# Performance work log

Measured on AMD Instinct MI355X. Metric: run time of the kernel, lower is better.

The kernel has to match this reference:

```python
import jax, jax.numpy as jnp
import numpy as np

HIDDEN = 512
HEADS = 8
NORM = 1.0 / np.sqrt(HIDDEN // HEADS)  # torch: 1/sqrt(tensor(dim_k)//head) = 1/8


def setup_inputs() -> dict:
    key = jax.random.key(0)
    ks = jax.random.split(key, 14)
    B, N, D = 2, 2048, HIDDEN
    s = 0.02
    d = {
        "x_re": jax.random.normal(ks[0], (B, N, D), dtype=jnp.float32),
        "x_im": jax.random.normal(ks[1], (B, N, D), dtype=jnp.float32),
    }
    names = ["Wq_re", "Wq_im", "bq_re", "bq_im",
             "Wk_re", "Wk_im", "bk_re", "bk_im",
             "Wv_re", "Wv_im", "bv_re", "bv_im"]
    for i, nm in enumerate(names):
        shape = (D, D) if nm.startswith("W") else (D,)
        d[nm] = jax.random.normal(ks[2 + i], shape, dtype=jnp.float32) * s
    return d


def reference(x_re, x_im,
              Wq_re, Wq_im, bq_re, bq_im,
              Wk_re, Wk_im, bk_re, bk_im,
              Wv_re, Wv_im, bv_re, bv_im):
    B, N, D = x_re.shape
    h, dk = HEADS, D // HEADS
    x = jax.lax.complex(x_re, x_im)
    Wq = jax.lax.complex(Wq_re, Wq_im); bq = jax.lax.complex(bq_re, bq_im)
    Wk = jax.lax.complex(Wk_re, Wk_im); bk = jax.lax.complex(bk_re, bk_im)
    Wv = jax.lax.complex(Wv_re, Wv_im); bv = jax.lax.complex(bv_re, bv_im)

    def proj(W, b):  # torch nn.Linear: x @ W.T + b, then split heads -> [B,h,N,dk]
        y = x @ W.T + b
        return y.reshape(B, N, h, dk).transpose(0, 2, 1, 3)

    q, k, v = proj(Wq, bq), proj(Wk, bk), proj(Wv, bv)
    # complex matmul (no conjugation, matching torch.matmul), scaled
    dist = jnp.einsum("bhnd,bhmd->bhnm", q, k) * NORM
    probs = jax.nn.softmax(jnp.abs(dist), axis=-1).astype(jnp.complex64)
    att = jnp.einsum("bhnm,bhmd->bhnd", probs, v)
    att = att.transpose(0, 2, 1, 3).reshape(B, N, D)
    # real-view output [B, N, D, 2]
    return jnp.stack([att.real, att.imag], axis=-1)
```

## Files before the change

### kernel.cpp

```cpp
#include <hip/hip_runtime.h>
#include <hip/hip_bf16.h>
#include <math.h>

#define B_ 2
#define N_ 2048
#define D_ 512
#define H_ 8
#define DK_ 64
#define M_ (B_ * N_)

typedef short s16x8 __attribute__((ext_vector_type(8)));
typedef short s16x4 __attribute__((ext_vector_type(4)));
typedef float fx4   __attribute__((ext_vector_type(4)));
typedef int   ix4   __attribute__((ext_vector_type(4)));

static __device__ __forceinline__ short f2bf(float f) {
    __hip_bfloat16 h = __float2bfloat16(f);
    return __builtin_bit_cast(short, h);
}
static __device__ __forceinline__ float bf2f(short s) {
    unsigned int u = ((unsigned int)(unsigned short)s) << 16;
    return __builtin_bit_cast(float, u);
}
static __device__ __forceinline__ float fexp2(float x) {
#if __has_builtin(__builtin_amdgcn_exp2f)
    return __builtin_amdgcn_exp2f(x);
#else
    return exp2f(x);
#endif
}
static __device__ __forceinline__ float fsqrt_(float x) {
#if __has_builtin(__builtin_amdgcn_sqrtf)
    return __builtin_amdgcn_sqrtf(x);
#else
    return sqrtf(x);
#endif
}
static __device__ __forceinline__ int pack_tr(float a, float b) {
    unsigned ua = __builtin_bit_cast(unsigned, a);
    unsigned ub = __builtin_bit_cast(unsigned, b);
    return (int)((ua >> 16) | (ub & 0xFFFF0000u));
}

#define MFMA16(a, b, c) __builtin_amdgcn_mfma_f32_16x16x32_bf16(a, b, c, 0, 0, 0)

#define C2_ 0.18033688f
#define M0_ 16.0f

__global__ __launch_bounds__(256, 2)
void qkproj_mfma(const float* __restrict__ xr, const float* __restrict__ xi,
                 const float* __restrict__ W0r, const float* __restrict__ W0i,
                 const float* __restrict__ b0r, const float* __restrict__ b0i,
                 const float* __restrict__ W1r, const float* __restrict__ W1i,
                 const float* __restrict__ b1r, const float* __restrict__ b1i,
                 short* __restrict__ o0r, short* __restrict__ o0i,
                 short* __restrict__ o1r, short* __restrict__ o1i)
{
    __shared__ short sA[2][128][40];
    __shared__ short sB[2][64][40];

    const int tid = threadIdx.x;
    const int w = tid >> 6, l = tid & 63, lg = l >> 4, lc = l & 15;
    const int wr = w >> 1, wc = w & 1;
    const int bn = blockIdx.x, bm = blockIdx.y, z = blockIdx.z;
    const float* Wr = z ? W1r : W0r;
    const float* Wi = z ? W1i : W0i;
    const float* br = z ? b1r : b0r;
    const float* bi = z ? b1i : b0i;
    short* outr = z ? o1r : o0r;
    short* outi = z ? o1i : o0i;

    const int srow = tid >> 3, scol = (tid & 7) * 4;
    int aoff = (bm * 128 + srow) * D_ + scol;
    int boff = (bn * 64 + srow) * D_ + scol;

    float4 rA[8], rB[4];
    auto issue = [&]() {
#pragma unroll
        for (int u = 0; u < 8; ++u) {
            const float* src = (u >= 4) ? xi : xr;
            rA[u] = *(const float4*)&src[aoff + (u & 3) * 32 * D_];
        }
#pragma unroll
        for (int u = 0; u < 4; ++u) {
            const float* src = (u >= 2) ? Wi : Wr;
            rB[u] = *(const float4*)&src[boff + (u & 1) * 32 * D_];
        }
        aoff += 32; boff += 32;
    };

    fx4 Cre[4][2], Cim[4][2];
#pragma unroll
    for (int mf = 0; mf < 4; ++mf)
#pragma unroll
        for (int nf = 0; nf < 2; ++nf)
#pragma unroll
            for (int j = 0; j < 4; ++j) { Cre[mf][nf][j] = 0.f; Cim[mf][nf][j] = 0.f; }

    issue();
    for (int k0 = 0; k0 < D_; k0 += 32) {
        __syncthreads();
#pragma unroll
        for (int u = 0; u < 8; ++u) {
            int comp = u >> 2, row = (u & 3) * 32 + srow;
            float vv[4] = {rA[u].x, rA[u].y, rA[u].z, rA[u].w};
            s16x4 hv;
#pragma unroll
            for (int q = 0; q < 4; ++q) hv[q] = f2bf(vv[q]);
            *(s16x4*)&sA[comp][row][scol] = hv;
        }
#pragma unroll
        for (int u = 0; u < 4; ++u) {
            int comp = u >> 1, row = (u & 1) * 32 + srow;
            float vv[4] = {rB[u].x, rB[u].y, rB[u].z, rB[u].w};
            s16x4 hv;
#pragma unroll
            for (int q = 0; q < 4; ++q) hv[q] = f2bf(vv[q]);
            *(s16x4*)&sB[comp][row][scol] = hv;
        }
        __syncthreads();
        if (k0 + 32 < D_) issue();

        s16x8 a[2][4];
#pragma unroll
        for (int comp = 0; comp < 2; ++comp)
#pragma unroll
            for (int mf = 0; mf < 4; ++mf)
                a[comp][mf] = *(const s16x8*)&sA[comp][wr * 64 + mf * 16 + lc][lg * 8];
        s16x8 bfr[2][2], bin[2];
#pragma unroll
        for (int comp = 0; comp < 2; ++comp)
#pragma unroll
            for (int nf = 0; nf < 2; ++nf)
                bfr[comp][nf] = *(const s16x8*)&sB[comp][wc * 32 + nf * 16 + lc][lg * 8];
#pragma unroll
        for (int nf = 0; nf < 2; ++nf) bin[nf] = bfr[1][nf] ^ (short)0x8000;

        __builtin_amdgcn_s_setprio(1);
#pragma unroll
        for (int mf = 0; mf < 4; ++mf)
#pragma unroll
            for (int nf = 0; nf < 2; ++nf) {
                Cre[mf][nf] = MFMA16(a[0][mf], bfr[0][nf], Cre[mf][nf]);
                Cre[mf][nf] = MFMA16(a[1][mf], bin[nf],    Cre[mf][nf]);
                Cim[mf][nf] = MFMA16(a[0][mf], bfr[1][nf], Cim[mf][nf]);
                Cim[mf][nf] = MFMA16(a[1][mf], bfr[0][nf], Cim[mf][nf]);
            }
        __builtin_amdgcn_s_setprio(0);
    }

    const int bb = (bm * 128) >> 11;
#pragma unroll
    for (int nf = 0; nf < 2; ++nf) {
        const int c = bn * 64 + wc * 32 + nf * 16 + lc;
        const float brv = br[c], biv = bi[c];
        const int h = c >> 6, dd = c & 63;
        const int n00 = (bm * 128 + wr * 64 + lg * 4) & (N_ - 1);
        size_t obase = (((size_t)(bb * H_ + h) * N_) + n00) * DK_ + dd;
#pragma unroll
        for (int mf = 0; mf < 4; ++mf)
#pragma unroll
            for (int j = 0; j < 4; ++j) {
                size_t o = obase + (size_t)(mf * 16 + j) * DK_;
                outr[o] = f2bf(Cre[mf][nf][j] + brv);
                outi[o] = f2bf(Cim[mf][nf][j] + biv);
            }
    }
}

__global__ __launch_bounds__(256, 2)
void vproj_mfma(const float* __restrict__ xr, const float* __restrict__ xi,
                const float* __restrict__ Wr, const float* __restrict__ Wi,
                const float* __restrict__ br, const float* __restrict__ bi,
                short* __restrict__ outr, short* __restrict__ outi)
{
    __shared__ short sA[2][2][64][40];
    __shared__ short sB[2][2][64][40];

    const int tid = threadIdx.x;
    const int w = tid >> 6, l = tid & 63, lg = l >> 4, lc = l & 15;
    const int wr = w >> 1, wc = w & 1;
    const int bn = blockIdx.x, bm = blockIdx.y;

    const int srow = tid >> 3, scol = (tid & 7) * 4;
    int aoff = (bm * 64 + srow) * D_ + scol;
    int boff = (bn * 64 + srow) * D_ + scol;

    float4 rA[4], rB[4];
    auto issue = [&]() {
#pragma unroll
        for (int u = 0; u < 4; ++u) {
            const float* src = (u >= 2) ? xi : xr;
            rA[u] = *(const float4*)&src[aoff + (u & 1) * 32 * D_];
        }
#pragma unroll
        for (int u = 0; u < 4; ++u) {
            const float* src = (u >= 2) ? Wi : Wr;
            rB[u] = *(const float4*)&src[boff + (u & 1) * 32 * D_];
        }
        aoff += 32; boff += 32;
    };

    fx4 Cre[2][2], Cim[2][2];
#pragma unroll
    for (int mf = 0; mf < 2; ++mf)
#pragma unroll
        for (int nf = 0; nf < 2; ++nf)
#pragma unroll
            for (int j = 0; j < 4; ++j) { Cre[mf][nf][j] = 0.f; Cim[mf][nf][j] = 0.f; }

    issue();
    for (int k0 = 0; k0 < D_; k0 += 32) {
        __syncthreads();
#pragma unroll
        for (int u = 0; u < 4; ++u) {
            int comp = u >> 1, row = (u & 1) * 32 + srow;
            float vv[4] = {rA[u].x, rA[u].y, rA[u].z, rA[u].w};
            s16x4 hv, lv;
#pragma unroll
            for (int q = 0; q < 4; ++q) {
                short hh = f2bf(vv[q]);
                hv[q] = hh;
                lv[q] = f2bf(vv[q] - bf2f(hh));
            }
            *(s16x4*)&sA[comp][0][row][scol] = hv;
            *(s16x4*)&sA[comp][1][row][scol] = lv;
        }
#pragma unroll
        for (int u = 0; u < 4; ++u) {
            int comp = u >> 1, row = (u & 1) * 32 + srow;
            float vv[4] = {rB[u].x, rB[u].y, rB[u].z, rB[u].w};
            s16x4 hv, lv;
#pragma unroll
            for (int q = 0; q < 4; ++q) {
                short hh = f2bf(vv[q]);
                hv[q] = hh;
                lv[q] = f2bf(vv[q] - bf2f(hh));
            }
            *(s16x4*)&sB[comp][0][row][scol] = hv;
            *(s16x4*)&sB[comp][1][row][scol] = lv;
        }
        __syncthreads();
        if (k0 + 32 < D_) issue();

        s16x8 a[2][2][2];
#pragma unroll
        for (int comp = 0; comp < 2; ++comp)
#pragma unroll
            for (int s = 0; s < 2; ++s)
#pragma unroll
                for (int mf = 0; mf < 2; ++mf)
                    a[comp][s][mf] = *(const s16x8*)&sA[comp][s][wr * 32 + mf * 16 + lc][lg * 8];
        s16x8 bfr[2][2][2], bin[2][2];
#pragma unroll
        for (int comp = 0; comp < 2; ++comp)
#pragma unroll
            for (int s = 0; s < 2; ++s)
#pragma unroll
                for (int nf = 0; nf < 2; ++nf)
                    bfr[comp][s][nf] = *(const s16x8*)&sB[comp][s][wc * 32 + nf * 16 + lc][lg * 8];
#pragma unroll
        for (int s = 0; s < 2; ++s)
#pragma unroll
            for (int nf = 0; nf < 2; ++nf)
                bin[s][nf] = bfr[1][s][nf] ^ (short)0x8000;

        __builtin_amdgcn_s_setprio(1);
#pragma unroll
        for (int mf = 0; mf < 2; ++mf)
#pragma unroll
            for (int nf = 0; nf < 2; ++nf) {
                fx4 cr = Cre[mf][nf], ci = Cim[mf][nf];
                cr = MFMA16(a[0][0][mf], bfr[0][0][nf], cr);
                cr = MFMA16(a[1][0][mf], bin[0][nf],    cr);
                ci = MFMA16(a[0][0][mf], bfr[1][0][nf], ci);
                ci = MFMA16(a[1][0][mf], bfr[0][0][nf], ci);
                cr = MFMA16(a[0][0][mf], bfr[0][1][nf], cr);
                cr = MFMA16(a[0][1][mf], bfr[0][0][nf], cr);
                cr = MFMA16(a[1][0][mf], bin[1][nf],    cr);
                cr = MFMA16(a[1][1][mf], bin[0][nf],    cr);
                ci = MFMA16(a[0][0][mf], bfr[1][1][nf], ci);
                ci = MFMA16(a[0][1][mf], bfr[1][0][nf], ci);
                ci = MFMA16(a[1][0][mf], bfr[0][1][nf], ci);
                ci = MFMA16(a[1][1][mf], bfr[0][0][nf], ci);
                Cre[mf][nf] = cr; Cim[mf][nf] = ci;
            }
        __builtin_amdgcn_s_setprio(0);
    }

    const int bb = (bm * 64) >> 11;
#pragma unroll
    for (int nf = 0; nf < 2; ++nf) {
        const int c = bn * 64 + wc * 32 + nf * 16 + lc;
        const float brv = br[c], biv = bi[c];
        const int h = c >> 6, dd = c & 63;
#pragma unroll
        for (int mf = 0; mf < 2; ++mf) {
            int m0 = bm * 64 + wr * 32 + mf * 16 + lg * 4;
            int n0 = m0 & (N_ - 1);
            s16x4 pr, pi;
#pragma unroll
            for (int j = 0; j < 4; ++j) {
                pr[j] = f2bf(Cre[mf][nf][j] + brv);
                pi[j] = f2bf(Cim[mf][nf][j] + biv);
            }
            size_t o = (((size_t)(bb * H_ + h) * DK_) + dd) * N_ + n0;
            *(s16x4*)&outr[o] = pr;
            *(s16x4*)&outi[o] = pi;
        }
    }
}

#define NT_ (N_ / 64)
#define NR_ (NT_ / 2)

static __device__ __forceinline__ int swz8(int row, int slot) {
    return (slot + (row & 7) + 2 * ((row >> 3) & 3)) & 7;
}

__global__ __launch_bounds__(512, 2)
void attn_mfma(const short* __restrict__ qr, const short* __restrict__ qi,
               const short* __restrict__ kr, const short* __restrict__ ki,
               const short* __restrict__ vtr, const short* __restrict__ vti,
               float* __restrict__ out)
{
    __shared__ short sK [2][2][2][64][64];
    __shared__ short sVt[2][2][2][64][64];

    const int tid = threadIdx.x;
    const int w = tid >> 6, l = tid & 63, lg = l >> 4, lc = l & 15;
    const int kg = w & 1, qw = w >> 1;

    const int dlin = blockIdx.y * 16 + blockIdx.x;
    const int xcd = dlin & 7, slot = dlin >> 3;
    const int bh = xcd * 2 + (slot >> 4);
    const int qt = slot & 15;
    const int b = bh >> 3, h = bh & 7;

    s16x8 Qr[2][2], Qi_[2][2], Qin[2][2];
#pragma unroll
    for (int qh = 0; qh < 2; ++qh) {
        size_t base = ((size_t)bh * N_ + (size_t)qt * 128 + qw * 32 + qh * 16 + lc) * DK_ + lg * 8;
#pragma unroll
        for (int c = 0; c < 2; ++c) {
            Qr[qh][c]  = *(const s16x8*)&qr[base + c * 32];
            Qi_[qh][c] = *(const s16x8*)&qi[base + c * 32];
            Qin[qh][c] = Qi_[qh][c] ^ (short)0x8000;
        }
    }

    s16x8 onesf;
#pragma unroll
    for (int u = 0; u < 8; ++u) onesf[u] = (short)0x3F80;

    fx4 o_re[2][4], o_im[2][4], o_l[2];
#pragma unroll
    for (int qh = 0; qh < 2; ++qh) {
#pragma unroll
        for (int dt = 0; dt < 4; ++dt)
#pragma unroll
            for (int j = 0; j < 4; ++j) { o_re[qh][dt][j] = 0.f; o_im[qh][dt][j] = 0.f; }
#pragma unroll
        for (int j = 0; j < 4; ++j) o_l[qh][j] = 0.f;
    }

    const int rS = ((lc >> 2) << 3) | (lc & 3);
    const int bqs = lg + (lc & 3) + 2 * (lc >> 2);
    const int bvs = lg + (lc & 7) + 2 * (lc >> 3);

    const int srow = tid >> 3, cs = tid & 7;
    const int sw = swz8(srow, cs) * 8;
    int koff = bh * (N_ * DK_) + srow * DK_ + cs * 8;
    int voff = bh * (DK_ * N_) + srow * N_ + cs * 8;

    s16x8 rgK[2][2], rgV[2][2];
    auto issue = [&]() {
#pragma unroll
        for (int g = 0; g < 2; ++g) {
            rgK[g][0] = *(const s16x8*)&kr [koff + g * 64 * DK_];
            rgK[g][1] = *(const s16x8*)&ki [koff + g * 64 * DK_];
            rgV[g][0] = *(const s16x8*)&vtr[voff + g * 64];
            rgV[g][1] = *(const s16x8*)&vti[voff + g * 64];
        }
        koff += 128 * DK_; voff += 128;
    };
    auto stage = [&](int nb) {
#pragma unroll
        for (int g = 0; g < 2; ++g)
#pragma unroll
            for (int comp = 0; comp < 2; ++comp) {
                *(s16x8*)&sK [nb][g][comp][srow][sw] = rgK[g][comp];
                *(s16x8*)&sVt[nb][g][comp][srow][sw] = rgV[g][comp];
            }
    };

    issue();
    stage(0);
    for (int r = 0; r < NR_; ++r) {
        const int cb = r & 1;
        __syncthreads();
        if (r + 1 < NR_) issue();

        fx4 are[2][4], aim[2][4];
#pragma unroll
        for (int qh = 0; qh < 2; ++qh)
#pragma unroll
            for (int t = 0; t < 4; ++t)
#pragma unroll
                for (int j = 0; j < 4; ++j) { are[qh][t][j] = 0.f; aim[qh][t][j] = 0.f; }

        __builtin_amdgcn_s_setprio(1);
#pragma unroll
        for (int t = 0; t < 4; ++t) {
            const int row = rS + ((t & 1) << 2) + ((t >> 1) << 5);
#pragma unroll
            for (int c = 0; c < 2; ++c) {
                const int sl = ((bqs + 4 * ((c + t) & 1)) & 7) * 8;
                s16x8 Krf = *(const s16x8*)&sK[cb][kg][0][row][sl];
                s16x8 Kif = *(const s16x8*)&sK[cb][kg][1][row][sl];
#pragma unroll
                for (int qh = 0; qh < 2; ++qh) {
                    are[qh][t] = MFMA16(Krf, Qr[qh][c],  are[qh][t]);
                    are[qh][t] = MFMA16(Kif, Qin[qh][c], are[qh][t]);
                    aim[qh][t] = MFMA16(Kif, Qr[qh][c],  aim[qh][t]);
                    aim[qh][t] = MFMA16(Krf, Qi_[qh][c], aim[qh][t]);
                }
            }
        }
        __builtin_amdgcn_s_setprio(0);

        s16x8 Pf[2][2];
#pragma unroll
        for (int qh = 0; qh < 2; ++qh) {
            ix4 w0, w1;
#pragma unroll
            for (int t = 0; t < 4; ++t) {
                float p[4];
#pragma unroll
                for (int j = 0; j < 4; ++j) {
                    float u2 = fmaf(are[qh][t][j], are[qh][t][j], aim[qh][t][j] * aim[qh][t][j]);
                    p[j] = fexp2(fmaf(C2_, fsqrt_(u2), -M0_));
                }
                int d0 = pack_tr(p[0], p[1]);
                int d1 = pack_tr(p[2], p[3]);
                if (t == 0)      { w0[0] = d0; w0[1] = d1; }
                else if (t == 1) { w0[2] = d0; w0[3] = d1; }
                else if (t == 2) { w1[0] = d0; w1[1] = d1; }
                else             { w1[2] = d0; w1[3] = d1; }
            }
            Pf[qh][0] = __builtin_bit_cast(s16x8, w0);
            Pf[qh][1] = __builtin_bit_cast(s16x8, w1);
        }

        __builtin_amdgcn_s_setprio(1);
#pragma unroll
        for (int qh = 0; qh < 2; ++qh) {
            o_l[qh] = MFMA16(Pf[qh][0], onesf, o_l[qh]);
            o_l[qh] = MFMA16(Pf[qh][1], onesf, o_l[qh]);
        }
#pragma unroll
        for (int dt = 0; dt < 4; ++dt) {
            const int d = dt * 16 + lc;
            const int s0 = ((bvs + 4 * dt) & 7) * 8;
            const int s1 = ((bvs + 4 * dt + 4) & 7) * 8;
            s16x8 Vr0 = *(const s16x8*)&sVt[cb][kg][0][d][s0];
            s16x8 Vi0 = *(const s16x8*)&sVt[cb][kg][1][d][s0];
            s16x8 Vr1 = *(const s16x8*)&sVt[cb][kg][0][d][s1];
            s16x8 Vi1 = *(const s16x8*)&sVt[cb][kg][1][d][s1];
#pragma unroll
            for (int qh = 0; qh < 2; ++qh) {
                o_re[qh][dt] = MFMA16(Pf[qh][0], Vr0, o_re[qh][dt]);
                o_im[qh][dt] = MFMA16(Pf[qh][0], Vi0, o_im[qh][dt]);
                o_re[qh][dt] = MFMA16(Pf[qh][1], Vr1, o_re[qh][dt]);
                o_im[qh][dt] = MFMA16(Pf[qh][1], Vi1, o_im[qh][dt]);
            }
        }
        __builtin_amdgcn_s_setprio(0);

        if (r + 1 < NR_) stage(cb ^ 1);
    }

    float* red = (float*)&sK[0][0][0][0][0];
    float2* po = (float2*)out;
#pragma unroll
    for (int qh = 0; qh < 2; ++qh) {
        __syncthreads();
        if (kg == 1) {
            const int base = (qw * 64 + l) * 37;
#pragma unroll
            for (int dt = 0; dt < 4; ++dt)
#pragma unroll
                for (int j = 0; j < 4; ++j) {
                    red[base + dt * 8 + j * 2 + 0] = o_re[qh][dt][j];
                    red[base + dt * 8 + j * 2 + 1] = o_im[qh][dt][j];
                }
#pragma unroll
            for (int j = 0; j < 4; ++j) red[base + 32 + j] = o_l[qh][j];
        }
        __syncthreads();
        if (kg == 0) {
            const int base = (qw * 64 + l) * 37;
            float inv[4];
#pragma unroll
            for (int j = 0; j < 4; ++j)
                inv[j] = 1.f / (o_l[qh][j] + red[base + 32 + j]);
#pragma unroll
            for (int dt = 0; dt < 4; ++dt)
#pragma unroll
                for (int j = 0; j < 4; ++j) {
                    float re = o_re[qh][dt][j] + red[base + dt * 8 + j * 2 + 0];
                    float im = o_im[qh][dt][j] + red[base + dt * 8 + j * 2 + 1];
                    int n  = qt * 128 + qw * 32 + qh * 16 + lg * 4 + j;
                    int dg = h * 64 + dt * 16 + lc;
                    po[((size_t)b * N_ + n) * D_ + dg] =
                        make_float2(re * inv[j], im * inv[j]);
                }
        }
    }
}

extern "C" void kernel_launch(void* const* d_in, const int* in_sizes, int n_in,
                              void* d_out, int out_size, void* d_ws, size_t ws_size,
                              hipStream_t stream)
{
    const float* xr = (const float*)d_in[0];
    const float* xi = (const float*)d_in[1];
    const float* Wq_r = (const float*)d_in[2];
    const float* Wq_i = (const float*)d_in[3];
    const float* bq_r = (const float*)d_in[4];
    const float* bq_i = (const float*)d_in[5];
    const float* Wk_r = (const float*)d_in[6];
    const float* Wk_i = (const float*)d_in[7];
    const float* bk_r = (const float*)d_in[8];
    const float* bk_i = (const float*)d_in[9];
    const float* Wv_r = (const float*)d_in[10];
    const float* Wv_i = (const float*)d_in[11];
    const float* bv_r = (const float*)d_in[12];
    const float* bv_i = (const float*)d_in[13];

    short* ws = (short*)d_ws;
    const size_t SZ = (size_t)B_ * H_ * N_ * DK_;
    short* qr_  = ws + 0 * SZ;
    short* qi_  = ws + 1 * SZ;
    short* kr_  = ws + 2 * SZ;
    short* ki_  = ws + 3 * SZ;
    short* vtr_ = ws + 4 * SZ;
    short* vti_ = ws + 5 * SZ;

    dim3 qkgrid(D_ / 64, M_ / 128, 2);
    qkproj_mfma<<<qkgrid, 256, 0, stream>>>(xr, xi,
                                            Wq_r, Wq_i, bq_r, bq_i,
                                            Wk_r, Wk_i, bk_r, bk_i,
                                            qr_, qi_, kr_, ki_);
    dim3 vgrid(D_ / 64, M_ / 64);
    vproj_mfma<<<vgrid, 256, 0, stream>>>(xr, xi, Wv_r, Wv_i, bv_r, bv_i, vtr_, vti_);

    dim3 agrid(16, 16);
    attn_mfma<<<agrid, 512, 0, stream>>>(qr_, qi_, kr_, ki_, vtr_, vti_, (float*)d_out);
}
```

Baseline: 120.7 us.

## Software-pipeline QK^T of next tile with softmax and PV of previous tile

Restructures the attention main loop into a skewed pipeline. The K-tile score MFMAs for iteration r are interleaved with the exp/pack of iteration r-1's magnitudes and its PV MFMAs, with K and V loads and staging split and offset by one iteration. A prologue and epilogue handle the first score tile and the final PV. The aim is to overlap transcendental VALU work with MFMA work to hide softmax latency, at the cost of extra live registers (the u2 array) and more complex buffer indexing.

After: 161.0 us. 33.5% more time.

```diff
diff --git a/kernel.cpp b/kernel.cpp
--- a/kernel.cpp
+++ b/kernel.cpp
@@ -374,33 +374,44 @@
     int voff = bh * (DK_ * N_) + srow * N_ + cs * 8;
 
     s16x8 rgK[2][2], rgV[2][2];
-    auto issue = [&]() {
+    auto issueK = [&]() {
 #pragma unroll
         for (int g = 0; g < 2; ++g) {
-            rgK[g][0] = *(const s16x8*)&kr [koff + g * 64 * DK_];
-            rgK[g][1] = *(const s16x8*)&ki [koff + g * 64 * DK_];
+            rgK[g][0] = *(const s16x8*)&kr[koff + g * 64 * DK_];
+            rgK[g][1] = *(const s16x8*)&ki[koff + g * 64 * DK_];
+        }
+        koff += 128 * DK_;
+    };
+    auto issueV = [&]() {
+#pragma unroll
+        for (int g = 0; g < 2; ++g) {
             rgV[g][0] = *(const s16x8*)&vtr[voff + g * 64];
             rgV[g][1] = *(const s16x8*)&vti[voff + g * 64];
         }
-        koff += 128 * DK_; voff += 128;
+        voff += 128;
     };
-    auto stage = [&](int nb) {
+    auto stageK = [&](int nb) {
 #pragma unroll
         for (int g = 0; g < 2; ++g)
 #pragma unroll
-            for (int comp = 0; comp < 2; ++comp) {
-                *(s16x8*)&sK [nb][g][comp][srow][sw] = rgK[g][comp];
+            for (int comp = 0; comp < 2; ++comp)
+                *(s16x8*)&sK[nb][g][comp][srow][sw] = rgK[g][comp];
+    };
+    auto stageV = [&](int nb) {
+#pragma unroll
+        for (int g = 0; g < 2; ++g)
+#pragma unroll
+            for (int comp = 0; comp < 2; ++comp)
                 *(s16x8*)&sVt[nb][g][comp][srow][sw] = rgV[g][comp];
-            }
     };
 
-    issue();
-    stage(0);
-    for (int r = 0; r < NR_; ++r) {
-        const int cb = r & 1;
-        __syncthreads();
-        if (r + 1 < NR_) issue();
-
+    fx4 u2[2][4];
+
+    issueK(); issueV();
+    stageK(0); stageV(0);
+    issueK(); issueV();
+    __syncthreads();
+    {
         fx4 are[2][4], aim[2][4];
 #pragma unroll
         for (int qh = 0; qh < 2; ++qh)
@@ -408,7 +419,6 @@
             for (int t = 0; t < 4; ++t)
 #pragma unroll
                 for (int j = 0; j < 4; ++j) { are[qh][t][j] = 0.f; aim[qh][t][j] = 0.f; }
-
         __builtin_amdgcn_s_setprio(1);
 #pragma unroll
         for (int t = 0; t < 4; ++t) {
@@ -416,8 +426,8 @@
 #pragma unroll
             for (int c = 0; c < 2; ++c) {
                 const int sl = ((bqs + 4 * ((c + t) & 1)) & 7) * 8;
-                s16x8 Krf = *(const s16x8*)&sK[cb][kg][0][row][sl];
-                s16x8 Kif = *(const s16x8*)&sK[cb][kg][1][row][sl];
+                s16x8 Krf = *(const s16x8*)&sK[0][kg][0][row][sl];
+                s16x8 Kif = *(const s16x8*)&sK[0][kg][1][row][sl];
 #pragma unroll
                 for (int qh = 0; qh < 2; ++qh) {
                     are[qh][t] = MFMA16(Krf, Qr[qh][c],  are[qh][t]);
@@ -428,30 +438,74 @@
             }
         }
         __builtin_amdgcn_s_setprio(0);
-
-        s16x8 Pf[2][2];
-#pragma unroll
-        for (int qh = 0; qh < 2; ++qh) {
-            ix4 w0, w1;
-#pragma unroll
-            for (int t = 0; t < 4; ++t) {
+#pragma unroll
+        for (int qh = 0; qh < 2; ++qh)
+#pragma unroll
+            for (int t = 0; t < 4; ++t)
+#pragma unroll
+                for (int j = 0; j < 4; ++j)
+                    u2[qh][t][j] = fmaf(are[qh][t][j], are[qh][t][j],
+                                        aim[qh][t][j] * aim[qh][t][j]);
+        stageK(1);
+    }
+
+    for (int r = 1; r < NR_; ++r) {
+        const int cb = r & 1;
+        __syncthreads();
+        if (r + 1 < NR_) issueK();
+        stageV(cb);
+        if (r + 1 < NR_) issueV();
+
+        fx4 are[2][4], aim[2][4];
+#pragma unroll
+        for (int qh = 0; qh < 2; ++qh)
+#pragma unroll
+            for (int t = 0; t < 4; ++t)
+#pragma unroll
+                for (int j = 0; j < 4; ++j) { are[qh][t][j] = 0.f; aim[qh][t][j] = 0.f; }
+
+        ix4 wA[2], wB[2];
+        __builtin_amdgcn_s_setprio(1);
+#pragma unroll
+        for (int t = 0; t < 4; ++t) {
+            const int row = rS + ((t & 1) << 2) + ((t >> 1) << 5);
+#pragma unroll
+            for (int c = 0; c < 2; ++c) {
+                const int sl = ((bqs + 4 * ((c + t) & 1)) & 7) * 8;
+                s16x8 Krf = *(const s16x8*)&sK[cb][kg][0][row][sl];
+                s16x8 Kif = *(const s16x8*)&sK[cb][kg][1][row][sl];
+#pragma unroll
+                for (int qh = 0; qh < 2; ++qh) {
+                    are[qh][t] = MFMA16(Krf, Qr[qh][c],  are[qh][t]);
+                    are[qh][t] = MFMA16(Kif, Qin[qh][c], are[qh][t]);
+                    aim[qh][t] = MFMA16(Kif, Qr[qh][c],  aim[qh][t]);
+                    aim[qh][t] = MFMA16(Krf, Qi_[qh][c], aim[qh][t]);
+                }
+            }
+#pragma unroll
+            for (int qh = 0; qh < 2; ++qh) {
                 float p[4];
 #pragma unroll
-                for (int j = 0; j < 4; ++j) {
-                    float u2 = fmaf(are[qh][t][j], are[qh][t][j], aim[qh][t][j] * aim[qh][t][j]);
-                    p[j] = fexp2(fmaf(C2_, fsqrt_(u2), -M0_));
-                }
+                for (int j = 0; j < 4; ++j)
+                    p[j] = fexp2(fmaf(C2_, fsqrt_(u2[qh][t][j]), -M0_));
                 int d0 = pack_tr(p[0], p[1]);
                 int d1 = pack_tr(p[2], p[3]);
-                if (t == 0)      { w0[0] = d0; w0[1] = d1; }
-                else if (t == 1) { w0[2] = d0; w0[3] = d1; }
-                else if (t == 2) { w1[0] = d0; w1[1] = d1; }
-                else             { w1[2] = d0; w1[3] = d1; }
-            }
-            Pf[qh][0] = __builtin_bit_cast(s16x8, w0);
-            Pf[qh][1] = __builtin_bit_cast(s16x8, w1);
-        }
-
+                if (t == 0)      { wA[qh][0] = d0; wA[qh][1] = d1; }
+                else if (t == 1) { wA[qh][2] = d0; wA[qh][3] = d1; }
+                else if (t == 2) { wB[qh][0] = d0; wB[qh][1] = d1; }
+                else             { wB[qh][2] = d0; wB[qh][3] = d1; }
+            }
+        }
+        __builtin_amdgcn_s_setprio(0);
+
+        s16x8 Pf[2][2];
+#pragma unroll
+        for (int qh = 0; qh < 2; ++qh) {
+            Pf[qh][0] = __builtin_bit_cast(s16x8, wA[qh]);
+            Pf[qh][1] = __builtin_bit_cast(s16x8, wB[qh]);
+        }
+
+        const int vb = cb ^ 1;
         __builtin_amdgcn_s_setprio(1);
 #pragma unroll
         for (int qh = 0; qh < 2; ++qh) {
@@ -463,10 +517,10 @@
             const int d = dt * 16 + lc;
             const int s0 = ((bvs + 4 * dt) & 7) * 8;
             const int s1 = ((bvs + 4 * dt + 4) & 7) * 8;
-            s16x8 Vr0 = *(const s16x8*)&sVt[cb][kg][0][d][s0];
-            s16x8 Vi0 = *(const s16x8*)&sVt[cb][kg][1][d][s0];
-            s16x8 Vr1 = *(const s16x8*)&sVt[cb][kg][0][d][s1];
-            s16x8 Vi1 = *(const s16x8*)&sVt[cb][kg][1][d][s1];
+            s16x8 Vr0 = *(const s16x8*)&sVt[vb][kg][0][d][s0];
+            s16x8 Vi0 = *(const s16x8*)&sVt[vb][kg][1][d][s0];
+            s16x8 Vr1 = *(const s16x8*)&sVt[vb][kg][0][d][s1];
+            s16x8 Vi1 = *(const s16x8*)&sVt[vb][kg][1][d][s1];
 #pragma unroll
             for (int qh = 0; qh < 2; ++qh) {
                 o_re[qh][dt] = MFMA16(Pf[qh][0], Vr0, o_re[qh][dt]);
@@ -474,10 +528,67 @@
                 o_re[qh][dt] = MFMA16(Pf[qh][1], Vr1, o_re[qh][dt]);
                 o_im[qh][dt] = MFMA16(Pf[qh][1], Vi1, o_im[qh][dt]);
             }
+#pragma unroll
+            for (int qh = 0; qh < 2; ++qh)
+#pragma unroll
+                for (int j = 0; j < 4; ++j)
+                    u2[qh][dt][j] = fmaf(are[qh][dt][j], are[qh][dt][j],
+                                         aim[qh][dt][j] * aim[qh][dt][j]);
         }
         __builtin_amdgcn_s_setprio(0);
 
-        if (r + 1 < NR_) stage(cb ^ 1);
+        if (r + 1 < NR_) stageK(cb ^ 1);
+    }
+
+    __syncthreads();
+    {
+        ix4 wA[2], wB[2];
+#pragma unroll
+        for (int t = 0; t < 4; ++t)
+#pragma unroll
+            for (int qh = 0; qh < 2; ++qh) {
+                float p[4];
+#pragma unroll
+                for (int j = 0; j < 4; ++j)
+                    p[j] = fexp2(fmaf(C2_, fsqrt_(u2[qh][t][j]), -M0_));
+                int d0 = pack_tr(p[0], p[1]);
+                int d1 = pack_tr(p[2], p[3]);
+                if (t == 0)      { wA[qh][0] = d0; wA[qh][1] = d1; }
+                else if (t == 1) { wA[qh][2] = d0; wA[qh][3] = d1; }
+                else if (t == 2) { wB[qh][0] = d0; wB[qh][1] = d1; }
+                else             { wB[qh][2] = d0; wB[qh][3] = d1; }
+            }
+        s16x8 Pf[2][2];
+#pragma unroll
+        for (int qh = 0; qh < 2; ++qh) {
+            Pf[qh][0] = __builtin_bit_cast(s16x8, wA[qh]);
+            Pf[qh][1] = __builtin_bit_cast(s16x8, wB[qh]);
+        }
+        const int vb = (NR_ - 1) & 1;
+        __builtin_amdgcn_s_setprio(1);
+#pragma unroll
+        for (int qh = 0; qh < 2; ++qh) {
+            o_l[qh] = MFMA16(Pf[qh][0], onesf, o_l[qh]);
+            o_l[qh] = MFMA16(Pf[qh][1], onesf, o_l[qh]);
+        }
+#pragma unroll
+        for (int dt = 0; dt < 4; ++dt) {
+            const int d = dt * 16 + lc;
+            const int s0 = ((bvs + 4 * dt) & 7) * 8;
+            const int s1 = ((bvs + 4 * dt + 4) & 7) * 8;
+            s16x8 Vr0 = *(const s16x8*)&sVt[vb][kg][0][d][s0];
+            s16x8 Vi0 = *(const s16x8*)&sVt[vb][kg][1][d][s0];
+            s16x8 Vr1 = *(const s16x8*)&sVt[vb][kg][0][d][s1];
+            s16x8 Vi1 = *(const s16x8*)&sVt[vb][kg][1][d][s1];
+#pragma unroll
+            for (int qh = 0; qh < 2; ++qh) {
+                o_re[qh][dt] = MFMA16(Pf[qh][0], Vr0, o_re[qh][dt]);
+                o_im[qh][dt] = MFMA16(Pf[qh][0], Vi0, o_im[qh][dt]);
+                o_re[qh][dt] = MFMA16(Pf[qh][1], Vr1, o_re[qh][dt]);
+                o_im[qh][dt] = MFMA16(Pf[qh][1], Vi1, o_im[qh][dt]);
+            }
+        }
+        __builtin_amdgcn_s_setprio(0);
     }
 
     float* red = (float*)&sK[0][0][0][0][0];
```

## Software-pipeline attention rounds: overlap QK of next block with PV of previous

Applied to the files above, without the earlier changes.

Restructures the attention main loop so that each round computes QK scores and softmax for the current key block while running the PV MFMAs for the previous block, using ping-pong probability registers (PfE/PfO). K and V loads and LDS staging are split and scheduled separately so V lags K by one round. The negated Q imaginary registers are dropped and replaced by negating K on the fly, which cuts register pressure at the cost of extra XORs per LDS read. The interleave is meant to hide softmax transcendental latency behind matrix work, but it adds live registers and relies on the unrolled pairing being correct when NR_ is even.

Result: slower. 127.4 us (+5.6%).

```diff
diff --git a/kernel.cpp b/kernel.cpp
--- a/kernel.cpp
+++ b/kernel.cpp
@@ -337,7 +337,7 @@
     const int qt = slot & 15;
     const int b = bh >> 3, h = bh & 7;
 
-    s16x8 Qr[2][2], Qi_[2][2], Qin[2][2];
+    s16x8 Qr[2][2], Qi_[2][2];
 #pragma unroll
     for (int qh = 0; qh < 2; ++qh) {
         size_t base = ((size_t)bh * N_ + (size_t)qt * 128 + qw * 32 + qh * 16 + lc) * DK_ + lg * 8;
@@ -345,7 +345,6 @@
         for (int c = 0; c < 2; ++c) {
             Qr[qh][c]  = *(const s16x8*)&qr[base + c * 32];
             Qi_[qh][c] = *(const s16x8*)&qi[base + c * 32];
-            Qin[qh][c] = Qi_[qh][c] ^ (short)0x8000;
         }
     }
 
@@ -374,111 +373,151 @@
     int voff = bh * (DK_ * N_) + srow * N_ + cs * 8;
 
     s16x8 rgK[2][2], rgV[2][2];
-    auto issue = [&]() {
+    auto issueK = [&]() {
 #pragma unroll
         for (int g = 0; g < 2; ++g) {
-            rgK[g][0] = *(const s16x8*)&kr [koff + g * 64 * DK_];
-            rgK[g][1] = *(const s16x8*)&ki [koff + g * 64 * DK_];
+            rgK[g][0] = *(const s16x8*)&kr[koff + g * 64 * DK_];
+            rgK[g][1] = *(const s16x8*)&ki[koff + g * 64 * DK_];
+        }
+        koff += 128 * DK_;
+    };
+    auto issueV = [&]() {
+#pragma unroll
+        for (int g = 0; g < 2; ++g) {
             rgV[g][0] = *(const s16x8*)&vtr[voff + g * 64];
             rgV[g][1] = *(const s16x8*)&vti[voff + g * 64];
         }
-        koff += 128 * DK_; voff += 128;
+        voff += 128;
     };
-    auto stage = [&](int nb) {
+    auto stageK = [&](int nb) {
 #pragma unroll
         for (int g = 0; g < 2; ++g)
 #pragma unroll
-            for (int comp = 0; comp < 2; ++comp) {
-                *(s16x8*)&sK [nb][g][comp][srow][sw] = rgK[g][comp];
+            for (int comp = 0; comp < 2; ++comp)
+                *(s16x8*)&sK[nb][g][comp][srow][sw] = rgK[g][comp];
+    };
+    auto stageV = [&](int nb) {
+#pragma unroll
+        for (int g = 0; g < 2; ++g)
+#pragma unroll
+            for (int comp = 0; comp < 2; ++comp)
                 *(s16x8*)&sVt[nb][g][comp][srow][sw] = rgV[g][comp];
-            }
     };
 
-    issue();
-    stage(0);
-    for (int r = 0; r < NR_; ++r) {
-        const int cb = r & 1;
-        __syncthreads();
-        if (r + 1 < NR_) issue();
-
-        fx4 are[2][4], aim[2][4];
-#pragma unroll
-        for (int qh = 0; qh < 2; ++qh)
-#pragma unroll
-            for (int t = 0; t < 4; ++t)
-#pragma unroll
-                for (int j = 0; j < 4; ++j) { are[qh][t][j] = 0.f; aim[qh][t][j] = 0.f; }
-
-        __builtin_amdgcn_s_setprio(1);
-#pragma unroll
-        for (int t = 0; t < 4; ++t) {
-            const int row = rS + ((t & 1) << 2) + ((t >> 1) << 5);
-#pragma unroll
-            for (int c = 0; c < 2; ++c) {
-                const int sl = ((bqs + 4 * ((c + t) & 1)) & 7) * 8;
-                s16x8 Krf = *(const s16x8*)&sK[cb][kg][0][row][sl];
-                s16x8 Kif = *(const s16x8*)&sK[cb][kg][1][row][sl];
-#pragma unroll
-                for (int qh = 0; qh < 2; ++qh) {
-                    are[qh][t] = MFMA16(Krf, Qr[qh][c],  are[qh][t]);
-                    are[qh][t] = MFMA16(Kif, Qin[qh][c], are[qh][t]);
-                    aim[qh][t] = MFMA16(Kif, Qr[qh][c],  aim[qh][t]);
-                    aim[qh][t] = MFMA16(Krf, Qi_[qh][c], aim[qh][t]);
-                }
-            }
-        }
-        __builtin_amdgcn_s_setprio(0);
-
-        s16x8 Pf[2][2];
-#pragma unroll
-        for (int qh = 0; qh < 2; ++qh) {
-            ix4 w0, w1;
-#pragma unroll
-            for (int t = 0; t < 4; ++t) {
-                float p[4];
-#pragma unroll
-                for (int j = 0; j < 4; ++j) {
-                    float u2 = fmaf(are[qh][t][j], are[qh][t][j], aim[qh][t][j] * aim[qh][t][j]);
-                    p[j] = fexp2(fmaf(C2_, fsqrt_(u2), -M0_));
-                }
-                int d0 = pack_tr(p[0], p[1]);
-                int d1 = pack_tr(p[2], p[3]);
-                if (t == 0)      { w0[0] = d0; w0[1] = d1; }
-                else if (t == 1) { w0[2] = d0; w0[3] = d1; }
-                else if (t == 2) { w1[0] = d0; w1[1] = d1; }
-                else             { w1[2] = d0; w1[3] = d1; }
-            }
-            Pf[qh][0] = __builtin_bit_cast(s16x8, w0);
-            Pf[qh][1] = __builtin_bit_cast(s16x8, w1);
-        }
-
-        __builtin_amdgcn_s_setprio(1);
-#pragma unroll
-        for (int qh = 0; qh < 2; ++qh) {
-            o_l[qh] = MFMA16(Pf[qh][0], onesf, o_l[qh]);
-            o_l[qh] = MFMA16(Pf[qh][1], onesf, o_l[qh]);
-        }
-#pragma unroll
-        for (int dt = 0; dt < 4; ++dt) {
-            const int d = dt * 16 + lc;
-            const int s0 = ((bvs + 4 * dt) & 7) * 8;
-            const int s1 = ((bvs + 4 * dt + 4) & 7) * 8;
-            s16x8 Vr0 = *(const s16x8*)&sVt[cb][kg][0][d][s0];
-            s16x8 Vi0 = *(const s16x8*)&sVt[cb][kg][1][d][s0];
-            s16x8 Vr1 = *(const s16x8*)&sVt[cb][kg][0][d][s1];
-            s16x8 Vi1 = *(const s16x8*)&sVt[cb][kg][1][d][s1];
-#pragma unroll
-            for (int qh = 0; qh < 2; ++qh) {
-                o_re[qh][dt] = MFMA16(Pf[qh][0], Vr0, o_re[qh][dt]);
-                o_im[qh][dt] = MFMA16(Pf[qh][0], Vi0, o_im[qh][dt]);
-                o_re[qh][dt] = MFMA16(Pf[qh][1], Vr1, o_re[qh][dt]);
-                o_im[qh][dt] = MFMA16(Pf[qh][1], Vi1, o_im[qh][dt]);
-            }
-        }
-        __builtin_amdgcn_s_setprio(0);
-
-        if (r + 1 < NR_) stage(cb ^ 1);
-    }
+    fx4 are[2][4], aim[2][4];
+    s16x8 PfE[2][2], PfO[2][2];
+
+#define QK_PAIR(CB_, T0_)                                                     \
+    _Pragma("unroll")                                                         \
+    for (int t = (T0_); t < (T0_) + 2; ++t) {                                 \
+        const int row = rS + ((t & 1) << 2) + ((t >> 1) << 5);                \
+        _Pragma("unroll")                                                     \
+        for (int c = 0; c < 2; ++c) {                                         \
+            const int sl = ((bqs + 4 * ((c + t) & 1)) & 7) * 8;               \
+            s16x8 Krf = *(const s16x8*)&sK[CB_][kg][0][row][sl];              \
+            s16x8 Kif = *(const s16x8*)&sK[CB_][kg][1][row][sl];              \
+            s16x8 Kin = Kif ^ (short)0x8000;                                  \
+            _Pragma("unroll")                                                 \
+            for (int qh = 0; qh < 2; ++qh) {                                  \
+                are[qh][t] = MFMA16(Krf, Qr[qh][c],  are[qh][t]);             \
+                are[qh][t] = MFMA16(Kin, Qi_[qh][c], are[qh][t]);             \
+                aim[qh][t] = MFMA16(Kif, Qr[qh][c],  aim[qh][t]);             \
+                aim[qh][t] = MFMA16(Krf, Qi_[qh][c], aim[qh][t]);             \
+            }                                                                 \
+        }                                                                     \
+    }
+
+#define SM_PAIR(T0_, PF_)                                                     \
+    _Pragma("unroll")                                                         \
+    for (int qh = 0; qh < 2; ++qh) {                                          \
+        ix4 wv;                                                               \
+        _Pragma("unroll")                                                     \
+        for (int t = (T0_); t < (T0_) + 2; ++t) {                             \
+            float p[4];                                                       \
+            _Pragma("unroll")                                                 \
+            for (int j = 0; j < 4; ++j) {                                     \
+                float u2v = fmaf(are[qh][t][j], are[qh][t][j],                \
+                                 aim[qh][t][j] * aim[qh][t][j]);              \
+                p[j] = fexp2(fmaf(C2_, fsqrt_(u2v), -M0_));                   \
+            }                                                                 \
+            wv[(t - (T0_)) * 2 + 0] = pack_tr(p[0], p[1]);                    \
+            wv[(t - (T0_)) * 2 + 1] = pack_tr(p[2], p[3]);                    \
+        }                                                                     \
+        PF_[qh][(T0_) >> 1] = __builtin_bit_cast(s16x8, wv);                  \
+    }
+
+#define PV_ALL(VB_, PF_)                                                      \
+    _Pragma("unroll")                                                         \
+    for (int qh = 0; qh < 2; ++qh) {                                          \
+        o_l[qh] = MFMA16(PF_[qh][0], onesf, o_l[qh]);                         \
+        o_l[qh] = MFMA16(PF_[qh][1], onesf, o_l[qh]);                         \
+    }                                                                         \
+    _Pragma("unroll")                                                         \
+    for (int dt = 0; dt < 4; ++dt) {                                          \
+        const int d = dt * 16 + lc;                                           \
+        const int s0 = ((bvs + 4 * dt) & 7) * 8;                              \
+        const int s1 = ((bvs + 4 * dt + 4) & 7) * 8;                          \
+        s16x8 Vr0 = *(const s16x8*)&sVt[VB_][kg][0][d][s0];                   \
+        s16x8 Vi0 = *(const s16x8*)&sVt[VB_][kg][1][d][s0];                   \
+        s16x8 Vr1 = *(const s16x8*)&sVt[VB_][kg][0][d][s1];                   \
+        s16x8 Vi1 = *(const s16x8*)&sVt[VB_][kg][1][d][s1];                   \
+        _Pragma("unroll")                                                     \
+        for (int qh = 0; qh < 2; ++qh) {                                      \
+            o_re[qh][dt] = MFMA16(PF_[qh][0], Vr0, o_re[qh][dt]);             \
+            o_im[qh][dt] = MFMA16(PF_[qh][0], Vi0, o_im[qh][dt]);             \
+            o_re[qh][dt] = MFMA16(PF_[qh][1], Vr1, o_re[qh][dt]);             \
+            o_im[qh][dt] = MFMA16(PF_[qh][1], Vi1, o_im[qh][dt]);             \
+        }                                                                     \
+    }
+
+#define ZERO_ACC()                                                            \
+    _Pragma("unroll")                                                         \
+    for (int qh = 0; qh < 2; ++qh)                                            \
+        _Pragma("unroll")                                                     \
+        for (int t = 0; t < 4; ++t)                                           \
+            _Pragma("unroll")                                                 \
+            for (int j = 0; j < 4; ++j) { are[qh][t][j] = 0.f; aim[qh][t][j] = 0.f; }
+
+#define ROUND(R_, PF_IN, PF_OUT) {                                            \
+    const int cb_ = (R_) & 1;                                                 \
+    __syncthreads();                                                          \
+    if ((R_) + 1 < NR_) issueK();                                             \
+    stageV(cb_);                                                              \
+    if ((R_) + 1 < NR_) issueV();                                             \
+    ZERO_ACC();                                                               \
+    __builtin_amdgcn_s_setprio(1);                                            \
+    QK_PAIR(cb_, 0)                                                           \
+    QK_PAIR(cb_, 2)                                                           \
+    SM_PAIR(0, PF_OUT)                                                        \
+    PV_ALL(cb_ ^ 1, PF_IN)                                                    \
+    SM_PAIR(2, PF_OUT)                                                        \
+    __builtin_amdgcn_s_setprio(0);                                            \
+    if ((R_) + 1 < NR_) stageK(((R_) + 1) & 1);                               \
+}
+
+    issueK(); issueV();
+    stageK(0); stageV(0);
+    issueK(); issueV();
+    __syncthreads();
+    ZERO_ACC();
+    __builtin_amdgcn_s_setprio(1);
+    QK_PAIR(0, 0)
+    QK_PAIR(0, 2)
+    SM_PAIR(0, PfE)
+    SM_PAIR(2, PfE)
+    __builtin_amdgcn_s_setprio(0);
+    stageK(1);
+
+    ROUND(1, PfE, PfO)
+    for (int rr = 2; rr < NR_; rr += 2) {
+        ROUND(rr,     PfO, PfE)
+        ROUND(rr + 1, PfE, PfO)
+    }
+
+    __syncthreads();
+    __builtin_amdgcn_s_setprio(1);
+    PV_ALL(1, PfO)
+    __builtin_amdgcn_s_setprio(0);
 
     float* red = (float*)&sK[0][0][0][0][0];
     float2* po = (float2*)out;
@@ -517,6 +556,11 @@
                 }
         }
     }
+#undef QK_PAIR
+#undef SM_PAIR
+#undef PV_ALL
+#undef ZERO_ACC
+#undef ROUND
 }
 
 extern "C" void kernel_launch(void* const* d_in, const int* in_sizes, int n_in,
```

## Pre-convert inputs and weights to bf16 hi/lo in a separate pass

Applied to the files above, without the earlier changes.

Adds a cvt_prep kernel that converts x and the Q/K/V weights from fp32 into bf16 hi (and lo for the V path) buffers in workspace once. The projection kernels then load bf16 data directly instead of reloading fp32 and converting inside every tile. This is meant to remove redundant conversion work and halve the global load bytes in the GEMMs. In exchange it adds a kernel launch plus an extra round trip of the data through memory (fp32 read, bf16 write, bf16 read).

New measurement: 125.7 us. +4.2%, slower.

```diff
diff --git a/kernel.cpp b/kernel.cpp
--- a/kernel.cpp
+++ b/kernel.cpp
@@ -47,11 +47,51 @@
 #define C2_ 0.18033688f
 #define M0_ 16.0f
 
+__global__ __launch_bounds__(256)
+void cvt_prep(const float* __restrict__ xr, const float* __restrict__ xi,
+              const float* __restrict__ Wqr, const float* __restrict__ Wqi,
+              const float* __restrict__ Wkr, const float* __restrict__ Wki,
+              const float* __restrict__ Wvr, const float* __restrict__ Wvi,
+              short* __restrict__ xhr, short* __restrict__ xhi2,
+              short* __restrict__ xlr, short* __restrict__ xli,
+              short* __restrict__ wqhr, short* __restrict__ wqhi,
+              short* __restrict__ wkhr, short* __restrict__ wkhi,
+              short* __restrict__ wvhr, short* __restrict__ wvhi,
+              short* __restrict__ wvlr, short* __restrict__ wvli)
+{
+    const int seg = blockIdx.y;
+    const float* src; short* hi; short* lo; int n4;
+    switch (seg) {
+        case 0:  src = xr;  hi = xhr;  lo = xlr;    n4 = (M_ * D_) / 4; break;
+        case 1:  src = xi;  hi = xhi2; lo = xli;    n4 = (M_ * D_) / 4; break;
+        case 2:  src = Wvr; hi = wvhr; lo = wvlr;   n4 = (D_ * D_) / 4; break;
+        case 3:  src = Wvi; hi = wvhi; lo = wvli;   n4 = (D_ * D_) / 4; break;
+        case 4:  src = Wqr; hi = wqhr; lo = nullptr; n4 = (D_ * D_) / 4; break;
+        case 5:  src = Wqi; hi = wqhi; lo = nullptr; n4 = (D_ * D_) / 4; break;
+        case 6:  src = Wkr; hi = wkhr; lo = nullptr; n4 = (D_ * D_) / 4; break;
+        default: src = Wki; hi = wkhi; lo = nullptr; n4 = (D_ * D_) / 4; break;
+    }
+    for (int i = blockIdx.x * blockDim.x + threadIdx.x; i < n4;
+         i += gridDim.x * blockDim.x) {
+        float4 v = ((const float4*)src)[i];
+        float vv[4] = {v.x, v.y, v.z, v.w};
+        s16x4 hv, lv;
+#pragma unroll
+        for (int q = 0; q < 4; ++q) {
+            short hh = f2bf(vv[q]);
+            hv[q] = hh;
+            lv[q] = f2bf(vv[q] - bf2f(hh));
+        }
+        ((s16x4*)hi)[i] = hv;
+        if (lo) ((s16x4*)lo)[i] = lv;
+    }
+}
+
 __global__ __launch_bounds__(256, 2)
-void qkproj_mfma(const float* __restrict__ xr, const float* __restrict__ xi,
-                 const float* __restrict__ W0r, const float* __restrict__ W0i,
+void qkproj_mfma(const short* __restrict__ xhr, const short* __restrict__ xhi,
+                 const short* __restrict__ w0r, const short* __restrict__ w0i,
                  const float* __restrict__ b0r, const float* __restrict__ b0i,
-                 const float* __restrict__ W1r, const float* __restrict__ W1i,
+                 const short* __restrict__ w1r, const short* __restrict__ w1i,
                  const float* __restrict__ b1r, const float* __restrict__ b1i,
                  short* __restrict__ o0r, short* __restrict__ o0i,
                  short* __restrict__ o1r, short* __restrict__ o1i)
@@ -63,8 +103,8 @@
     const int w = tid >> 6, l = tid & 63, lg = l >> 4, lc = l & 15;
     const int wr = w >> 1, wc = w & 1;
     const int bn = blockIdx.x, bm = blockIdx.y, z = blockIdx.z;
-    const float* Wr = z ? W1r : W0r;
-    const float* Wi = z ? W1i : W0i;
+    const short* Wr = z ? w1r : w0r;
+    const short* Wi = z ? w1i : w0i;
     const float* br = z ? b1r : b0r;
     const float* bi = z ? b1i : b0i;
     short* outr = z ? o1r : o0r;
@@ -74,17 +114,17 @@
     int aoff = (bm * 128 + srow) * D_ + scol;
     int boff = (bn * 64 + srow) * D_ + scol;
 
-    float4 rA[8], rB[4];
+    s16x4 rA[8], rB[4];
     auto issue = [&]() {
 #pragma unroll
         for (int u = 0; u < 8; ++u) {
-            const float* src = (u >= 4) ? xi : xr;
-            rA[u] = *(const float4*)&src[aoff + (u & 3) * 32 * D_];
+            const short* src = (u >= 4) ? xhi : xhr;
+            rA[u] = *(const s16x4*)&src[aoff + (u & 3) * 32 * D_];
         }
 #pragma unroll
         for (int u = 0; u < 4; ++u) {
-            const float* src = (u >= 2) ? Wi : Wr;
-            rB[u] = *(const float4*)&src[boff + (u & 1) * 32 * D_];
+            const short* src = (u >= 2) ? Wi : Wr;
+            rB[u] = *(const s16x4*)&src[boff + (u & 1) * 32 * D_];
         }
         aoff += 32; boff += 32;
     };
@@ -103,20 +143,12 @@
 #pragma unroll
         for (int u = 0; u < 8; ++u) {
             int comp = u >> 2, row = (u & 3) * 32 + srow;
-            float vv[4] = {rA[u].x, rA[u].y, rA[u].z, rA[u].w};
-            s16x4 hv;
-#pragma unroll
-            for (int q = 0; q < 4; ++q) hv[q] = f2bf(vv[q]);
-            *(s16x4*)&sA[comp][row][scol] = hv;
+            *(s16x4*)&sA[comp][row][scol] = rA[u];
         }
 #pragma unroll
         for (int u = 0; u < 4; ++u) {
             int comp = u >> 1, row = (u & 1) * 32 + srow;
-            float vv[4] = {rB[u].x, rB[u].y, rB[u].z, rB[u].w};
-            s16x4 hv;
-#pragma unroll
-            for (int q = 0; q < 4; ++q) hv[q] = f2bf(vv[q]);
-            *(s16x4*)&sB[comp][row][scol] = hv;
+            *(s16x4*)&sB[comp][row][scol] = rB[u];
         }
         __syncthreads();
         if (k0 + 32 < D_) issue();
@@ -169,8 +201,10 @@
 }
 
 __global__ __launch_bounds__(256, 2)
-void vproj_mfma(const float* __restrict__ xr, const float* __restrict__ xi,
-                const float* __restrict__ Wr, const float* __restrict__ Wi,
+void vproj_mfma(const short* __restrict__ xhr, const short* __restrict__ xhi,
+                const short* __restrict__ xlr, const short* __restrict__ xli,
+                const short* __restrict__ whr, const short* __restrict__ whi,
+                const short* __restrict__ wlr, const short* __restrict__ wli,
                 const float* __restrict__ br, const float* __restrict__ bi,
                 short* __restrict__ outr, short* __restrict__ outi)
 {
@@ -186,17 +220,21 @@
     int aoff = (bm * 64 + srow) * D_ + scol;
     int boff = (bn * 64 + srow) * D_ + scol;
 
-    float4 rA[4], rB[4];
+    s16x4 rAh[4], rAl[4], rBh[4], rBl[4];
     auto issue = [&]() {
 #pragma unroll
         for (int u = 0; u < 4; ++u) {
-            const float* src = (u >= 2) ? xi : xr;
-            rA[u] = *(const float4*)&src[aoff + (u & 1) * 32 * D_];
+            const short* sh = (u >= 2) ? xhi : xhr;
+            const short* sl = (u >= 2) ? xli : xlr;
+            rAh[u] = *(const s16x4*)&sh[aoff + (u & 1) * 32 * D_];
+            rAl[u] = *(const s16x4*)&sl[aoff + (u & 1) * 32 * D_];
         }
 #pragma unroll
         for (int u = 0; u < 4; ++u) {
-            const float* src = (u >= 2) ? Wi : Wr;
-            rB[u] = *(const float4*)&src[boff + (u & 1) * 32 * D_];
+            const short* sh = (u >= 2) ? whi : whr;
+            const short* sl = (u >= 2) ? wli : wlr;
+            rBh[u] = *(const s16x4*)&sh[boff + (u & 1) * 32 * D_];
+            rBl[u] = *(const s16x4*)&sl[boff + (u & 1) * 32 * D_];
         }
         aoff += 32; boff += 32;
     };
@@ -215,30 +253,14 @@
 #pragma unroll
         for (int u = 0; u < 4; ++u) {
             int comp = u >> 1, row = (u & 1) * 32 + srow;
-            float vv[4] = {rA[u].x, rA[u].y, rA[u].z, rA[u].w};
-            s16x4 hv, lv;
-#pragma unroll
-            for (int q = 0; q < 4; ++q) {
-                short hh = f2bf(vv[q]);
-                hv[q] = hh;
-                lv[q] = f2bf(vv[q] - bf2f(hh));
-            }
-            *(s16x4*)&sA[comp][0][row][scol] = hv;
-            *(s16x4*)&sA[comp][1][row][scol] = lv;
+            *(s16x4*)&sA[comp][0][row][scol] = rAh[u];
+            *(s16x4*)&sA[comp][1][row][scol] = rAl[u];
         }
 #pragma unroll
         for (int u = 0; u < 4; ++u) {
             int comp = u >> 1, row = (u & 1) * 32 + srow;
-            float vv[4] = {rB[u].x, rB[u].y, rB[u].z, rB[u].w};
-            s16x4 hv, lv;
-#pragma unroll
-            for (int q = 0; q < 4; ++q) {
-                short hh = f2bf(vv[q]);
-                hv[q] = hh;
-                lv[q] = f2bf(vv[q] - bf2f(hh));
-            }
-            *(s16x4*)&sB[comp][0][row][scol] = hv;
-            *(s16x4*)&sB[comp][1][row][scol] = lv;
+            *(s16x4*)&sB[comp][0][row][scol] = rBh[u];
+            *(s16x4*)&sB[comp][1][row][scol] = rBl[u];
         }
         __syncthreads();
         if (k0 + 32 < D_) issue();
@@ -540,20 +562,42 @@
 
     short* ws = (short*)d_ws;
     const size_t SZ = (size_t)B_ * H_ * N_ * DK_;
+    const size_t WZ = (size_t)D_ * D_;
     short* qr_  = ws + 0 * SZ;
     short* qi_  = ws + 1 * SZ;
     short* kr_  = ws + 2 * SZ;
     short* ki_  = ws + 3 * SZ;
     short* vtr_ = ws + 4 * SZ;
     short* vti_ = ws + 5 * SZ;
+    short* xhr_ = ws + 6 * SZ;
+    short* xhi_ = ws + 7 * SZ;
+    short* xlr_ = ws + 8 * SZ;
+    short* xli_ = ws + 9 * SZ;
+    short* wb   = ws + 10 * SZ;
+    short* wqhr_ = wb + 0 * WZ;
+    short* wqhi_ = wb + 1 * WZ;
+    short* wkhr_ = wb + 2 * WZ;
+    short* wkhi_ = wb + 3 * WZ;
+    short* wvhr_ = wb + 4 * WZ;
+    short* wvhi_ = wb + 5 * WZ;
+    short* wvlr_ = wb + 6 * WZ;
+    short* wvli_ = wb + 7 * WZ;
+
+    dim3 pgrid(512, 8);
+    cvt_prep<<<pgrid, 256, 0, stream>>>(xr, xi, Wq_r, Wq_i, Wk_r, Wk_i, Wv_r, Wv_i,
+                                        xhr_, xhi_, xlr_, xli_,
+                                        wqhr_, wqhi_, wkhr_, wkhi_,
+                                        wvhr_, wvhi_, wvlr_, wvli_);
 
     dim3 qkgrid(D_ / 64, M_ / 128, 2);
-    qkproj_mfma<<<qkgrid, 256, 0, stream>>>(xr, xi,
-                                            Wq_r, Wq_i, bq_r, bq_i,
-                                            Wk_r, Wk_i, bk_r, bk_i,
+    qkproj_mfma<<<qkgrid, 256, 0, stream>>>(xhr_, xhi_,
+                                            wqhr_, wqhi_, bq_r, bq_i,
+                                            wkhr_, wkhi_, bk_r, bk_i,
                                             qr_, qi_, kr_, ki_);
     dim3 vgrid(D_ / 64, M_ / 64);
-    vproj_mfma<<<vgrid, 256, 0, stream>>>(xr, xi, Wv_r, Wv_i, bv_r, bv_i, vtr_, vti_);
+    vproj_mfma<<<vgrid, 256, 0, stream>>>(xhr_, xhi_, xlr_, xli_,
+                                          wvhr_, wvhi_, wvlr_, wvli_,
+                                          bv_r, bv_i, vtr_, vti_);
 
     dim3 agrid(16, 16);
     attn_mfma<<<agrid, 512, 0, stream>>>(qr_, qi_, kr_, ki_, vtr_, vti_, (float*)d_out);
```
